# Performance work log

Measured on AMD Instinct MI355X. Metric: run time of the kernel, lower is better.

## Reference

```python
import jax, jax.numpy as jnp
import numpy as np
from jax import lax

# Grid / layer constants matching init_kwargs
D, H, W = 41, 159, 159   # spatial_shape (chosen so (dim-K) % S == 0)
K = 3                    # kernel_size
S = 2                    # stride
CIN, COUT = 32, 64       # in_channels, out_channels
B = 2                    # batch_size
N_PER_BATCH = 75000      # active voxels per batch element (unique coords)


def setup_inputs() -> dict:
    # Unique active-voxel coordinates per batch (spconv assumes no duplicates).
    rng = np.random.default_rng(0)
    nvox = D * H * W
    rows = []
    for b in range(B):
        lin = rng.choice(nvox, size=N_PER_BATCH, replace=False)
        z = lin // (H * W)
        y = (lin // W) % H
        x = lin % W
        rows.append(np.stack([np.full(N_PER_BATCH, b), z, y, x], axis=1))
    coors = jnp.asarray(np.concatenate(rows, axis=0), dtype=jnp.int32)  # [N,4]

    key = jax.random.key(0)
    k1, k2, k3 = jax.random.split(key, 3)
    features = jax.random.normal(k1, (B * N_PER_BATCH, CIN), dtype=jnp.float32)
    # SparseConv3d weight (no bias): kernel [K,K,K,CIN,COUT] in DHWIO layout.
    w1 = (jax.random.normal(k2, (K, K, K, CIN, COUT), dtype=jnp.float32) * 0.05)
    # SparseInverseConv3d weight: transpose-conv mapping COUT -> CIN; stored in
    # forward-conv DHWIO layout [K,K,K,CIN,COUT] and applied via conv_transpose
    # with transpose_kernel=True (the exact adjoint of the forward conv op).
    w2 = (jax.random.normal(k3, (K, K, K, CIN, COUT), dtype=jnp.float32) * 0.05)
    return {"features": features, "coors": coors, "batch_size": B, "w1": w1, "w2": w2}


def reference(features, coors, batch_size, w1, w2):
    # Scatter active features into a dense NDHWC grid (equivalent to the sparse
    # tensor; SparseConv3d with bias=False gives identical values on active sites).
    b, z, y, x = coors[:, 0], coors[:, 1], coors[:, 2], coors[:, 3]
    dense = jnp.zeros((batch_size, D, H, W, CIN), features.dtype).at[b, z, y, x].set(features)
    # Mask of originally-active sites: SparseInverseConv3d (shared indice_key)
    # only produces outputs at these sites, and ToDense zeros everything else.
    mask = jnp.zeros((batch_size, D, H, W, 1), features.dtype).at[b, z, y, x].set(1.0)

    dn = ("NDHWC", "DHWIO", "NDHWC")
    # SparseConv3d(CIN->COUT, k=3, s=2): strided VALID conv.
    mid = lax.conv_general_dilated(dense, w1, (S, S, S), "VALID", dimension_numbers=dn)
    # SparseInverseConv3d(COUT->CIN): exact transpose of the forward conv's
    # gather/scatter pattern; recovers the original spatial shape.
    back = lax.conv_transpose(mid, w2, (S, S, S), "VALID", dimension_numbers=dn,
                              transpose_kernel=True)
    out = back * mask  # restrict to original active sites, zeros elsewhere
    return jnp.transpose(out, (0, 4, 1, 2, 3))  # ToDense returns NCDHW
```

## Files before the change

kernel.cpp:

```cpp
#include <hip/hip_runtime.h>

#define D_   41
#define H_   159
#define W_   159
#define MD   20
#define MH   79
#define MW   79
#define CIN  32
#define COUT 64
#define BATCH 2

#define NTAP 27
#define WLDS (NTAP * 16 * 64)

#define BLK   1024
#define WPB   (BLK / 64)

typedef unsigned int u32;

static __device__ __forceinline__ u32 bf16_rn(float x) {
    u32 u = __float_as_uint(x);
    return (u + 0x7fffu + ((u >> 16) & 1u)) >> 16;
}
static __device__ __forceinline__ float bf_lo(u32 p) { return __uint_as_float(p << 16); }
static __device__ __forceinline__ float bf_hi(u32 p) { return __uint_as_float(p & 0xffff0000u); }

__global__ void pack_kernel(const float* __restrict__ w1, const float* __restrict__ w2,
                            u32* __restrict__ w1p, u32* __restrict__ w2p) {
    int i = blockIdx.x * 256 + threadIdx.x;
    if (i >= WLDS) return;
    int k  = i & 3;
    int co = (i >> 2) & 63;
    int j4 = (i >> 8) & 3;
    int t  = i >> 10;
    int j  = j4 * 4 + k;
    int s0 = (t * 32 + 2 * j) * 64 + co;
    int s1 = (t * 32 + 2 * j + 1) * 64 + co;
    w1p[i] = bf16_rn(w1[s0]) | (bf16_rn(w1[s1]) << 16);
    w2p[i] = bf16_rn(w2[s0]) | (bf16_rn(w2[s1]) << 16);
}

__global__ void scatter_idx_kernel(const int* __restrict__ coors,
                                   int* __restrict__ idx, int n) {
    int i = blockIdx.x * blockDim.x + threadIdx.x;
    if (i >= n) return;
    int4 c = ((const int4*)coors)[i];
    idx[((c.x * D_ + c.y) * H_ + c.z) * W_ + c.w] = i;
}

#define LOADW(dst, base, t)                                        \
    {                                                              \
        const uint4* wq = (const uint4*)(base) + (t) * 256 + lane; \
        uint4 q0 = wq[0], q1 = wq[64], q2 = wq[128], q3 = wq[192]; \
        dst[0] = q0.x;  dst[1] = q0.y;  dst[2] = q0.z;  dst[3] = q0.w;   \
        dst[4] = q1.x;  dst[5] = q1.y;  dst[6] = q1.z;  dst[7] = q1.w;   \
        dst[8] = q2.x;  dst[9] = q2.y;  dst[10] = q2.z; dst[11] = q2.w;  \
        dst[12] = q3.x; dst[13] = q3.y; dst[14] = q3.z; dst[15] = q3.w;  \
    }

__global__ __launch_bounds__(BLK) void mid_kernel(const float* __restrict__ feat,
                                                  const int* __restrict__ idx,
                                                  const u32* __restrict__ w1p,
                                                  float* __restrict__ mid) {
    const int NV = BATCH * MD * MH * MW;
    int lane = threadIdx.x & 63;
    int wid  = threadIdx.x >> 6;
    int nw   = gridDim.x * WPB;
    int gw   = blockIdx.x * WPB + wid;
    int per  = (NV + nw - 1) / nw;
    int v0   = gw * per;
    int v1   = v0 + per; if (v1 > NV) v1 = NV;

    int l  = lane < NTAP ? lane : NTAP - 1;
    int kz = l / 9, kr = l % 9, ky = kr / 3, kx = kr % 3;

    auto probe = [&](int v) -> int {
        if (v >= v1 || lane >= NTAP) return -1;
        int xo = v % MW; int t0 = v / MW;
        int yo = t0 % MH; t0 /= MH;
        int zo = t0 % MD; int b = t0 / MD;
        return idx[((b * D_ + 2 * zo + kz) * H_ + 2 * yo + ky) * W_ + 2 * xo + kx];
    };

    int pA = probe(v0), pB = probe(v0 + 1);
    for (int v = v0; v < v1; v += 2) {
        int cA = pA, cB = pB;
        pA = probe(v + 2);
        pB = probe(v + 3);
        unsigned long long mA = __ballot(cA >= 0);
        unsigned long long mB = __ballot(cB >= 0);

        float a0 = 0.f, a1 = 0.f, b0 = 0.f, b1 = 0.f;
        while (mA | mB) {
            bool hA = mA != 0, hB = mB != 0;
            float4 fav[8], fbv[8];
            u32 wav[16], wbv[16];
            if (hA) {
                int t = (int)__builtin_ctzll(mA); mA &= mA - 1;
                int pp = __shfl(cA, t);
                const float4* f4 = (const float4*)(feat + (size_t)pp * CIN);
                #pragma unroll
                for (int q = 0; q < 8; ++q) fav[q] = f4[q];
                LOADW(wav, w1p, t)
            }
            if (hB) {
                int t = (int)__builtin_ctzll(mB); mB &= mB - 1;
                int pp = __shfl(cB, t);
                const float4* f4 = (const float4*)(feat + (size_t)pp * CIN);
                #pragma unroll
                for (int q = 0; q < 8; ++q) fbv[q] = f4[q];
                LOADW(wbv, w1p, t)
            }
            if (hA) {
                #pragma unroll
                for (int q = 0; q < 8; ++q) {
                    a0 = fmaf(fav[q].x, bf_lo(wav[2 * q + 0]), a0);
                    a1 = fmaf(fav[q].y, bf_hi(wav[2 * q + 0]), a1);
                    a0 = fmaf(fav[q].z, bf_lo(wav[2 * q + 1]), a0);
                    a1 = fmaf(fav[q].w, bf_hi(wav[2 * q + 1]), a1);
                }
            }
            if (hB) {
                #pragma unroll
                for (int q = 0; q < 8; ++q) {
                    b0 = fmaf(fbv[q].x, bf_lo(wbv[2 * q + 0]), b0);
                    b1 = fmaf(fbv[q].y, bf_hi(wbv[2 * q + 0]), b1);
                    b0 = fmaf(fbv[q].z, bf_lo(wbv[2 * q + 1]), b0);
                    b1 = fmaf(fbv[q].w, bf_hi(wbv[2 * q + 1]), b1);
                }
            }
        }
        mid[(size_t)v * COUT + lane] = a0 + a1;
        if (v + 1 < v1) mid[(size_t)(v + 1) * COUT + lane] = b0 + b1;
    }
}

#define BSTEP(MK, HALF)                                            \
    {                                                              \
        bool up = (lane & MK) != 0;                                \
        _Pragma("unroll")                                          \
        for (int k = 0; k < HALF; ++k) {                           \
            float send = up ? acc[k] : acc[k + HALF];              \
            float keep = up ? acc[k + HALF] : acc[k];              \
            acc[k] = keep + __shfl_xor(send, MK, 64);              \
        }                                                          \
    }

__global__ __launch_bounds__(BLK) void out_kernel(const int* __restrict__ coors,
                                                  const float* __restrict__ mid,
                                                  const u32* __restrict__ w2p,
                                                  float* __restrict__ compact, int n) {
    __shared__ u32 lw[WLDS];
    for (int i = threadIdx.x; i < WLDS; i += BLK) lw[i] = w2p[i];
    __syncthreads();

    int lane = threadIdx.x & 63;
    int wid  = threadIdx.x >> 6;
    int nw   = gridDim.x * WPB;
    int gw   = blockIdx.x * WPB + wid;
    int per  = (n + nw - 1) / nw;
    int i0   = gw * per;
    int i1   = i0 + per; if (i1 > n) i1 = n;

    int l  = lane < NTAP ? lane : NTAP - 1;
    int kz = l / 9, kr = l % 9, ky = kr / 3, kx = kr % 3;

    const int4* cvec = (const int4*)coors;
    int4 nc = make_int4(0, 0, 0, 0);
    if (i0 < i1) nc = cvec[i0];

    for (int i = i0; i < i1; ++i) {
        int4 c = nc;
        if (i + 1 < i1) nc = cvec[i + 1];
        int b = c.x, z = c.y, y = c.z, x = c.w;

        int zr = z - kz, yr = y - ky, xr = x - kx;
        bool ok = (lane < NTAP) &&
                  zr >= 0 && !(zr & 1) && (zr >> 1) < MD &&
                  yr >= 0 && !(yr & 1) && (yr >> 1) < MH &&
                  xr >= 0 && !(xr & 1) && (xr >> 1) < MW;
        int vv = ok ? ((b * MD + (zr >> 1)) * MH + (yr >> 1)) * MW + (xr >> 1) : -1;
        unsigned long long m = __ballot(ok);

        float acc[CIN];
        #pragma unroll
        for (int ci = 0; ci < CIN; ++ci) acc[ci] = 0.f;

        while (m) {
            int t0 = (int)__builtin_ctzll(m); m &= m - 1;
            bool h1 = (m != 0);
            int t1 = 0;
            if (h1) { t1 = (int)__builtin_ctzll(m); m &= m - 1; }

            int ve0 = __shfl(vv, t0);
            float mr0 = mid[(size_t)ve0 * COUT + lane];
            u32 wv0[16];
            LOADW(wv0, lw, t0)

            float mr1 = 0.f; u32 wv1[16];
            if (h1) {
                int ve1 = __shfl(vv, t1);
                mr1 = mid[(size_t)ve1 * COUT + lane];
                LOADW(wv1, lw, t1)
            }

            #pragma unroll
            for (int j = 0; j < 16; ++j) {
                acc[2 * j + 0] = fmaf(mr0, bf_lo(wv0[j]), acc[2 * j + 0]);
                acc[2 * j + 1] = fmaf(mr0, bf_hi(wv0[j]), acc[2 * j + 1]);
            }
            if (h1) {
                #pragma unroll
                for (int j = 0; j < 16; ++j) {
                    acc[2 * j + 0] = fmaf(mr1, bf_lo(wv1[j]), acc[2 * j + 0]);
                    acc[2 * j + 1] = fmaf(mr1, bf_hi(wv1[j]), acc[2 * j + 1]);
                }
            }
        }

        BSTEP(32, 16)
        BSTEP(16, 8)
        BSTEP(8, 4)
        BSTEP(4, 2)
        BSTEP(2, 1)
        float s = acc[0] + __shfl_xor(acc[0], 1, 64);
        if (!(lane & 1))
            compact[(size_t)i * CIN + (lane >> 1)] = s;
    }
}

__global__ __launch_bounds__(256) void expand_kernel(const int* __restrict__ idx,
                                                     const float* __restrict__ compact,
                                                     float* __restrict__ out) {
    const int HW    = H_ * W_;
    const int PLANE = D_ * HW;
    const int NVOX  = BATCH * PLANE;
    int g = blockIdx.x * 256 + threadIdx.x;
    if (g >= NVOX) return;

    int p   = idx[g];
    int b   = g / PLANE;
    int rem = g - b * PLANE;

    float r[CIN];
    if (p >= 0) {
        const float4* row = (const float4*)(compact + (size_t)p * CIN);
        #pragma unroll
        for (int q = 0; q < 8; ++q) {
            float4 v = row[q];
            r[4 * q + 0] = v.x; r[4 * q + 1] = v.y;
            r[4 * q + 2] = v.z; r[4 * q + 3] = v.w;
        }
    } else {
        #pragma unroll
        for (int q = 0; q < CIN; ++q) r[q] = 0.f;
    }

    float* o = out + (size_t)b * ((size_t)CIN * PLANE) + rem;
    #pragma unroll
    for (int ci = 0; ci < CIN; ++ci)
        __builtin_nontemporal_store(r[ci], o + (size_t)ci * PLANE);
}

extern "C" void kernel_launch(void* const* d_in, const int* in_sizes, int n_in,
                              void* d_out, int out_size, void* d_ws, size_t ws_size,
                              hipStream_t stream) {
    const float* feat  = (const float*)d_in[0];
    const int*   coors = (const int*)d_in[1];
    const float* w1    = (const float*)d_in[3];
    const float* w2    = (const float*)d_in[4];
    float*       out   = (float*)d_out;

    int n = in_sizes[0] / CIN;

    int*   idx      = (int*)d_ws;
    size_t idxBytes = (size_t)BATCH * D_ * H_ * W_ * sizeof(int);
    size_t midOff   = (idxBytes + 255) & ~(size_t)255;
    float* mid      = (float*)((char*)d_ws + midOff);
    size_t wOff     = midOff + (size_t)BATCH * MD * MH * MW * COUT * sizeof(float);
    wOff            = (wOff + 255) & ~(size_t)255;
    u32*   w1p      = (u32*)((char*)d_ws + wOff);
    u32*   w2p      = w1p + WLDS;
    float* compact  = (float*)(w2p + WLDS);

    (void)hipMemsetAsync(idx, 0xFF, idxBytes, stream);

    pack_kernel<<<(WLDS + 255) / 256, 256, 0, stream>>>(w1, w2, w1p, w2p);
    scatter_idx_kernel<<<(n + 255) / 256, 256, 0, stream>>>(coors, idx, n);

    mid_kernel<<<512, BLK, 0, stream>>>(feat, idx, w1p, mid);
    out_kernel<<<256, BLK, 0, stream>>>(coors, mid, w2p, compact, n);

    const int NVOX = BATCH * D_ * H_ * W_;
    expand_kernel<<<(NVOX + 255) / 256, 256, 0, stream>>>(idx, compact, out);
}
```

Measured before the change: 686.0 us.

## Switch to fp16 packed dot2 math with fp16 features, intermediates, and LDS weights

Converts weights and input features to packed fp16 and replaces scalar bf16-unpack FMAs with v_dot2 fp16 instructions in both conv kernels. The intermediate mid tensor is stored as fp16, halving its write and gather traffic, and mid_kernel now stages its weights in LDS with half the grid. out_kernel pairs two taps into one dot2 using byte permutes. This cuts ALU work and memory bandwidth but adds a feature-packing pass and fp16 range and precision risk.

```diff
diff --git a/kernel.cpp b/kernel.cpp
--- a/kernel.cpp
+++ b/kernel.cpp
@@ -17,13 +17,18 @@
 #define WPB   (BLK / 64)
 
 typedef unsigned int u32;
-
-static __device__ __forceinline__ u32 bf16_rn(float x) {
-    u32 u = __float_as_uint(x);
-    return (u + 0x7fffu + ((u >> 16) & 1u)) >> 16;
-}
-static __device__ __forceinline__ float bf_lo(u32 p) { return __uint_as_float(p << 16); }
-static __device__ __forceinline__ float bf_hi(u32 p) { return __uint_as_float(p & 0xffff0000u); }
+typedef unsigned short u16;
+typedef _Float16 f16;
+typedef f16 f16x2 __attribute__((ext_vector_type(2)));
+
+static __device__ __forceinline__ u32 f16pair(float a, float b) {
+    f16x2 h = { (f16)a, (f16)b };
+    return __builtin_bit_cast(u32, h);
+}
+static __device__ __forceinline__ float dot2(u32 a, u32 b, float c) {
+    return __builtin_amdgcn_fdot2(__builtin_bit_cast(f16x2, a),
+                                  __builtin_bit_cast(f16x2, b), c, false);
+}
 
 __global__ void pack_kernel(const float* __restrict__ w1, const float* __restrict__ w2,
                             u32* __restrict__ w1p, u32* __restrict__ w2p) {
@@ -36,8 +41,16 @@
     int j  = j4 * 4 + k;
     int s0 = (t * 32 + 2 * j) * 64 + co;
     int s1 = (t * 32 + 2 * j + 1) * 64 + co;
-    w1p[i] = bf16_rn(w1[s0]) | (bf16_rn(w1[s1]) << 16);
-    w2p[i] = bf16_rn(w2[s0]) | (bf16_rn(w2[s1]) << 16);
+    w1p[i] = f16pair(w1[s0], w1[s1]);
+    w2p[i] = f16pair(w2[s0], w2[s1]);
+}
+
+__global__ void featpack_kernel(const float* __restrict__ feat,
+                                u32* __restrict__ feat_h, int n16) {
+    int i = blockIdx.x * 256 + threadIdx.x;
+    if (i >= n16) return;
+    int p = i >> 4, j = i & 15;
+    feat_h[i] = f16pair(feat[p * CIN + 2 * j], feat[p * CIN + 2 * j + 1]);
 }
 
 __global__ void scatter_idx_kernel(const int* __restrict__ coors,
@@ -58,10 +71,14 @@
         dst[12] = q3.x; dst[13] = q3.y; dst[14] = q3.z; dst[15] = q3.w;  \
     }
 
-__global__ __launch_bounds__(BLK) void mid_kernel(const float* __restrict__ feat,
+__global__ __launch_bounds__(BLK) void mid_kernel(const u32* __restrict__ feat_h,
                                                   const int* __restrict__ idx,
                                                   const u32* __restrict__ w1p,
-                                                  float* __restrict__ mid) {
+                                                  u16* __restrict__ mid_h) {
+    __shared__ u32 lw[WLDS];
+    for (int i = threadIdx.x; i < WLDS; i += BLK) lw[i] = w1p[i];
+    __syncthreads();
+
     const int NV = BATCH * MD * MH * MW;
     int lane = threadIdx.x & 63;
     int wid  = threadIdx.x >> 6;
@@ -93,45 +110,51 @@
         float a0 = 0.f, a1 = 0.f, b0 = 0.f, b1 = 0.f;
         while (mA | mB) {
             bool hA = mA != 0, hB = mB != 0;
-            float4 fav[8], fbv[8];
+            uint4 fa0, fa1, fa2, fa3, fb0, fb1, fb2, fb3;
             u32 wav[16], wbv[16];
             if (hA) {
                 int t = (int)__builtin_ctzll(mA); mA &= mA - 1;
                 int pp = __shfl(cA, t);
-                const float4* f4 = (const float4*)(feat + (size_t)pp * CIN);
-                #pragma unroll
-                for (int q = 0; q < 8; ++q) fav[q] = f4[q];
-                LOADW(wav, w1p, t)
+                const uint4* f4 = (const uint4*)(feat_h + (size_t)pp * 16);
+                fa0 = f4[0]; fa1 = f4[1]; fa2 = f4[2]; fa3 = f4[3];
+                LOADW(wav, lw, t)
             }
             if (hB) {
                 int t = (int)__builtin_ctzll(mB); mB &= mB - 1;
                 int pp = __shfl(cB, t);
-                const float4* f4 = (const float4*)(feat + (size_t)pp * CIN);
-                #pragma unroll
-                for (int q = 0; q < 8; ++q) fbv[q] = f4[q];
-                LOADW(wbv, w1p, t)
+                const uint4* f4 = (const uint4*)(feat_h + (size_t)pp * 16);
+                fb0 = f4[0]; fb1 = f4[1]; fb2 = f4[2]; fb3 = f4[3];
+                LOADW(wbv, lw, t)
             }
             if (hA) {
-                #pragma unroll
-                for (int q = 0; q < 8; ++q) {
-                    a0 = fmaf(fav[q].x, bf_lo(wav[2 * q + 0]), a0);
-                    a1 = fmaf(fav[q].y, bf_hi(wav[2 * q + 0]), a1);
-                    a0 = fmaf(fav[q].z, bf_lo(wav[2 * q + 1]), a0);
-                    a1 = fmaf(fav[q].w, bf_hi(wav[2 * q + 1]), a1);
-                }
+                a0 = dot2(fa0.x, wav[0],  a0);  a1 = dot2(fa0.y, wav[1],  a1);
+                a0 = dot2(fa0.z, wav[2],  a0);  a1 = dot2(fa0.w, wav[3],  a1);
+                a0 = dot2(fa1.x, wav[4],  a0);  a1 = dot2(fa1.y, wav[5],  a1);
+                a0 = dot2(fa1.z, wav[6],  a0);  a1 = dot2(fa1.w, wav[7],  a1);
+                a0 = dot2(fa2.x, wav[8],  a0);  a1 = dot2(fa2.y, wav[9],  a1);
+                a0 = dot2(fa2.z, wav[10], a0);  a1 = dot2(fa2.w, wav[11], a1);
+                a0 = dot2(fa3.x, wav[12], a0);  a1 = dot2(fa3.y, wav[13], a1);
+                a0 = dot2(fa3.z, wav[14], a0);  a1 = dot2(fa3.w, wav[15], a1);
             }
             if (hB) {
-                #pragma unroll
-                for (int q = 0; q < 8; ++q) {
-                    b0 = fmaf(fbv[q].x, bf_lo(wbv[2 * q + 0]), b0);
-                    b1 = fmaf(fbv[q].y, bf_hi(wbv[2 * q + 0]), b1);
-                    b0 = fmaf(fbv[q].z, bf_lo(wbv[2 * q + 1]), b0);
-                    b1 = fmaf(fbv[q].w, bf_hi(wbv[2 * q + 1]), b1);
-                }
-            }
-        }
-        mid[(size_t)v * COUT + lane] = a0 + a1;
-        if (v + 1 < v1) mid[(size_t)(v + 1) * COUT + lane] = b0 + b1;
+                b0 = dot2(fb0.x, wbv[0],  b0);  b1 = dot2(fb0.y, wbv[1],  b1);
+                b0 = dot2(fb0.z, wbv[2],  b0);  b1 = dot2(fb0.w, wbv[3],  b1);
+                b0 = dot2(fb1.x, wbv[4],  b0);  b1 = dot2(fb1.y, wbv[5],  b1);
+                b0 = dot2(fb1.z, wbv[6],  b0);  b1 = dot2(fb1.w, wbv[7],  b1);
+                b0 = dot2(fb2.x, wbv[8],  b0);  b1 = dot2(fb2.y, wbv[9],  b1);
+                b0 = dot2(fb2.z, wbv[10], b0);  b1 = dot2(fb2.w, wbv[11], b1);
+                b0 = dot2(fb3.x, wbv[12], b0);  b1 = dot2(fb3.y, wbv[13], b1);
+                b0 = dot2(fb3.z, wbv[14], b0);  b1 = dot2(fb3.w, wbv[15], b1);
+            }
+        }
+        {
+            f16 hv = (f16)(a0 + a1);
+            mid_h[(size_t)v * COUT + lane] = __builtin_bit_cast(u16, hv);
+        }
+        if (v + 1 < v1) {
+            f16 hv = (f16)(b0 + b1);
+            mid_h[(size_t)(v + 1) * COUT + lane] = __builtin_bit_cast(u16, hv);
+        }
     }
 }
 
@@ -147,7 +170,7 @@
     }
 
 __global__ __launch_bounds__(BLK) void out_kernel(const int* __restrict__ coors,
-                                                  const float* __restrict__ mid,
+                                                  const u16* __restrict__ mid_h,
                                                   const u32* __restrict__ w2p,
                                                   float* __restrict__ compact, int n) {
     __shared__ u32 lw[WLDS];
@@ -193,28 +216,24 @@
             if (h1) { t1 = (int)__builtin_ctzll(m); m &= m - 1; }
 
             int ve0 = __shfl(vv, t0);
-            float mr0 = mid[(size_t)ve0 * COUT + lane];
-            u32 wv0[16];
-            LOADW(wv0, lw, t0)
-
-            float mr1 = 0.f; u32 wv1[16];
+            u32 mr0 = mid_h[(size_t)ve0 * COUT + lane];
+            u32 mr1 = 0;
             if (h1) {
                 int ve1 = __shfl(vv, t1);
-                mr1 = mid[(size_t)ve1 * COUT + lane];
-                LOADW(wv1, lw, t1)
-            }
+                mr1 = mid_h[(size_t)ve1 * COUT + lane];
+            }
+            u32 mrp = mr0 | (mr1 << 16);
+
+            u32 wv0[16], wv1[16];
+            LOADW(wv0, lw, t0)
+            LOADW(wv1, lw, t1)
 
             #pragma unroll
             for (int j = 0; j < 16; ++j) {
-                acc[2 * j + 0] = fmaf(mr0, bf_lo(wv0[j]), acc[2 * j + 0]);
-                acc[2 * j + 1] = fmaf(mr0, bf_hi(wv0[j]), acc[2 * j + 1]);
-            }
-            if (h1) {
-                #pragma unroll
-                for (int j = 0; j < 16; ++j) {
-                    acc[2 * j + 0] = fmaf(mr1, bf_lo(wv1[j]), acc[2 * j + 0]);
-                    acc[2 * j + 1] = fmaf(mr1, bf_hi(wv1[j]), acc[2 * j + 1]);
-                }
+                u32 wlo = __builtin_amdgcn_perm(wv1[j], wv0[j], 0x05040100u);
+                u32 whi = __builtin_amdgcn_perm(wv1[j], wv0[j], 0x07060302u);
+                acc[2 * j + 0] = dot2(mrp, wlo, acc[2 * j + 0]);
+                acc[2 * j + 1] = dot2(mrp, whi, acc[2 * j + 1]);
             }
         }
 
@@ -276,20 +295,22 @@
     int*   idx      = (int*)d_ws;
     size_t idxBytes = (size_t)BATCH * D_ * H_ * W_ * sizeof(int);
     size_t midOff   = (idxBytes + 255) & ~(size_t)255;
-    float* mid      = (float*)((char*)d_ws + midOff);
-    size_t wOff     = midOff + (size_t)BATCH * MD * MH * MW * COUT * sizeof(float);
+    u16*   mid_h    = (u16*)((char*)d_ws + midOff);
+    size_t wOff     = midOff + (size_t)BATCH * MD * MH * MW * COUT * sizeof(u16);
     wOff            = (wOff + 255) & ~(size_t)255;
     u32*   w1p      = (u32*)((char*)d_ws + wOff);
     u32*   w2p      = w1p + WLDS;
     float* compact  = (float*)(w2p + WLDS);
+    u32*   feat_h   = (u32*)(compact + (size_t)n * CIN);
 
     (void)hipMemsetAsync(idx, 0xFF, idxBytes, stream);
 
     pack_kernel<<<(WLDS + 255) / 256, 256, 0, stream>>>(w1, w2, w1p, w2p);
+    featpack_kernel<<<(n * 16 + 255) / 256, 256, 0, stream>>>(feat, feat_h, n * 16);
     scatter_idx_kernel<<<(n + 255) / 256, 256, 0, stream>>>(coors, idx, n);
 
-    mid_kernel<<<512, BLK, 0, stream>>>(feat, idx, w1p, mid);
-    out_kernel<<<256, BLK, 0, stream>>>(coors, mid, w2p, compact, n);
+    mid_kernel<<<256, BLK, 0, stream>>>(feat_h, idx, w1p, mid_h);
+    out_kernel<<<256, BLK, 0, stream>>>(coors, mid_h, w2p, compact, n);
 
     const int NVOX = BATCH * D_ * H_ * W_;
     expand_kernel<<<(NVOX + 255) / 256, 256, 0, stream>>>(idx, compact, out);
```

After: 561.2 us. 18.2% less time.
